# Optimization experiments

Hardware: AMD Instinct MI355X
Metric: run time of the kernel (lower is better)

## Reference

```python
import jax, jax.numpy as jnp
import numpy as np

EMBED_DIM = 1024
NUM_HEADS = 16
HEAD_DIM = EMBED_DIM // NUM_HEADS
LN_EPS = 1e-5


def setup_inputs() -> dict:
    key = jax.random.key(0)
    ks = jax.random.split(key, 10)
    B, S, D = 1, 4096, EMBED_DIM
    s = 1.0 / np.sqrt(D)
    inp = {
        'input': jax.random.normal(ks[0], (B, S, D), dtype=jnp.float32),
        'Wq': jax.random.normal(ks[1], (D, D), dtype=jnp.float32) * s,
        'bq': jnp.zeros((D,), dtype=jnp.float32),
        'Wk': jax.random.normal(ks[2], (D, D), dtype=jnp.float32) * s,
        'bk': jnp.zeros((D,), dtype=jnp.float32),
        'Wv': jax.random.normal(ks[3], (D, D), dtype=jnp.float32) * s,
        'bv': jnp.zeros((D,), dtype=jnp.float32),
        'Wo': jax.random.normal(ks[4], (D, D), dtype=jnp.float32) * s,
        'bo': jnp.zeros((D,), dtype=jnp.float32),
        'ln_gamma': jnp.ones((D,), dtype=jnp.float32),
        'ln_beta': jnp.zeros((D,), dtype=jnp.float32),
    }
    return inp


def reference(input, Wq, bq, Wk, bk, Wv, bv, Wo, bo, ln_gamma, ln_beta):
    B, S, D = input.shape
    H, Hd = NUM_HEADS, HEAD_DIM
    # projections (torch Linear: x @ W.T + b)
    q = input @ Wq.T + bq
    k = input @ Wk.T + bk
    v = input @ Wv.T + bv
    # [B, H, S, Hd]
    q = q.reshape(B, S, H, Hd).transpose(0, 2, 1, 3)
    k = k.reshape(B, S, H, Hd).transpose(0, 2, 1, 3)
    v = v.reshape(B, S, H, Hd).transpose(0, 2, 1, 3)
    scores = jnp.einsum('bhqd,bhkd->bhqk', q, k) / jnp.sqrt(jnp.float32(Hd))
    causal = jnp.tril(jnp.ones((S, S), dtype=bool))  # [S, S]
    scores = jnp.where(causal[None, None, :, :], scores, -jnp.inf)
    attn = jax.nn.softmax(scores, axis=-1)  # stable (max-subtract) internally
    out = jnp.einsum('bhqk,bhkd->bhqd', attn, v)
    out = out.transpose(0, 2, 1, 3).reshape(B, S, D)
    out = out @ Wo.T + bo
    out = out + input
    # LayerNorm
    mu = jnp.mean(out, axis=-1, keepdims=True)
    var = jnp.var(out, axis=-1, keepdims=True)
    normed = (out - mu) * jax.lax.rsqrt(var + LN_EPS)
    return normed * ln_gamma + ln_beta
```

## Files before the change

### kernel.cpp

```cpp
#include <hip/hip_runtime.h>
#include <hip/hip_bf16.h>

typedef float floatx4 __attribute__((ext_vector_type(4)));
typedef short short8 __attribute__((ext_vector_type(8)));

#define S_LEN 4096
#define D_DIM 1024
#define NHEAD 16
#define SCALE_LOG2 0.1803368801111204f

__device__ __forceinline__ void gload_lds16(const void* g, void* l) {
  __builtin_amdgcn_global_load_lds(
      (const __attribute__((address_space(1))) unsigned int*)g,
      (__attribute__((address_space(3))) unsigned int*)l, 16, 0, 0);
}

__device__ __forceinline__ unsigned short f2bf_bits(float f) {
  __hip_bfloat16 h = __float2bfloat16(f);
  return __builtin_bit_cast(unsigned short, h);
}

__global__ __launch_bounds__(256) void cvt_all(const float* __restrict__ x,
                                               const float* __restrict__ w0,
                                               const float* __restrict__ w1,
                                               const float* __restrict__ w2,
                                               const float* __restrict__ w3,
                                               unsigned short* __restrict__ xo,
                                               unsigned short* __restrict__ o0,
                                               unsigned short* __restrict__ o1,
                                               unsigned short* __restrict__ o2,
                                               unsigned short* __restrict__ o3) {
  const int bid = blockIdx.x;
  const float* in;
  unsigned short* out;
  int i;
  if (bid < 4096) {
    in = x;
    out = xo;
    i = bid * 256 + threadIdx.x;
  } else {
    const int which = (bid - 4096) >> 10;
    in = which == 0 ? w0 : which == 1 ? w1 : which == 2 ? w2 : w3;
    out = which == 0 ? o0 : which == 1 ? o1 : which == 2 ? o2 : o3;
    i = ((bid - 4096) & 1023) * 256 + threadIdx.x;
  }
  float4 v = reinterpret_cast<const float4*>(in)[i];
  ushort4 u;
  u.x = f2bf_bits(v.x);
  u.y = f2bf_bits(v.y);
  u.z = f2bf_bits(v.z);
  u.w = f2bf_bits(v.w);
  reinterpret_cast<ushort4*>(out)[i] = u;
}

__global__ __launch_bounds__(256) void gemm_qkv(const unsigned short* __restrict__ A,
                                                const unsigned short* __restrict__ WqB,
                                                const unsigned short* __restrict__ WkB,
                                                const unsigned short* __restrict__ WvB,
                                                const float* __restrict__ bq,
                                                const float* __restrict__ bk,
                                                const float* __restrict__ bv,
                                                unsigned short* __restrict__ Qo,
                                                unsigned short* __restrict__ Ko,
                                                unsigned short* __restrict__ VTo) {
  __shared__ __align__(16) unsigned short As[2][128 * 32];
  __shared__ __align__(16) unsigned short Bs[2][128 * 32];
  const int K = 1024, N = 1024, M = 4096;
  const int tid = threadIdx.x;
  const int wave = tid >> 6, lane = tid & 63;
  const int seg = blockIdx.y >> 3;
  const int m0 = blockIdx.x * 128, n0 = (blockIdx.y & 7) * 128;
  const unsigned short* B = seg == 0 ? WqB : seg == 1 ? WkB : WvB;
  const float* bias = seg == 0 ? bq : seg == 1 ? bk : bv;
  const int wr = wave >> 1, wc = wave & 1;

  floatx4 acc[4][4] = {};
  const unsigned short* Ab = A + (size_t)m0 * K;
  const unsigned short* Bb = B + (size_t)n0 * K;
  const int srow = lane >> 2, scol = (lane & 3) * 8;
  const int aRow = lane & 15, kOff = (lane >> 4) * 8;

  auto stage = [&](int buf, int k0) {
#pragma unroll
    for (int i = 0; i < 2; ++i) {
      const int c = wave * 2 + i;
      const int row = c * 16 + srow;
      gload_lds16(Ab + (size_t)row * K + k0 + scol, &As[buf][c * 512]);
      gload_lds16(Bb + (size_t)row * K + k0 + scol, &Bs[buf][c * 512]);
    }
  };

  stage(0, 0);
  int buf = 0;
  for (int k0 = 0; k0 < K; k0 += 32, buf ^= 1) {
    asm volatile("s_waitcnt vmcnt(0)" ::: "memory");
    __builtin_amdgcn_s_barrier();
    if (k0 + 32 < K) stage(buf ^ 1, k0 + 32);
    short8 af[4], bfg[4];
#pragma unroll
    for (int f = 0; f < 4; ++f) {
      af[f] =
          *reinterpret_cast<const short8*>(&As[buf][(wr * 64 + f * 16 + aRow) * 32 + kOff]);
      bfg[f] =
          *reinterpret_cast<const short8*>(&Bs[buf][(wc * 64 + f * 16 + aRow) * 32 + kOff]);
    }
#pragma unroll
    for (int fm = 0; fm < 4; ++fm)
#pragma unroll
      for (int fn = 0; fn < 4; ++fn)
        acc[fm][fn] =
            __builtin_amdgcn_mfma_f32_16x16x32_bf16(af[fm], bfg[fn], acc[fm][fn], 0, 0, 0);
  }

  const int rb = (lane >> 4) * 4, cl = lane & 15;
  const float osc = seg == 0 ? SCALE_LOG2 : 1.0f;
#pragma unroll
  for (int fm = 0; fm < 4; ++fm)
#pragma unroll
    for (int fn = 0; fn < 4; ++fn)
#pragma unroll
      for (int r = 0; r < 4; ++r) {
        const int row = m0 + wr * 64 + fm * 16 + rb + r;
        const int col = n0 + wc * 64 + fn * 16 + cl;
        const float v = (acc[fm][fn][r] + bias[col]) * osc;
        if (seg == 0)
          Qo[(size_t)row * N + col] = f2bf_bits(v);
        else if (seg == 1)
          Ko[(size_t)row * N + col] = f2bf_bits(v);
        else
          VTo[(size_t)col * M + row] = f2bf_bits(v);
      }
}

__global__ __launch_bounds__(256) void gemm_o(const unsigned short* __restrict__ A,
                                              const unsigned short* __restrict__ B,
                                              const float* __restrict__ bias,
                                              const float* __restrict__ resid,
                                              float* __restrict__ C) {
  __shared__ __align__(16) unsigned short As[2][64 * 32];
  __shared__ __align__(16) unsigned short Bs[2][128 * 32];
  const int K = 1024, N = 1024;
  const int tid = threadIdx.x;
  const int wave = tid >> 6, lane = tid & 63;
  const int m0 = blockIdx.x * 64, n0 = blockIdx.y * 128;
  const int wr = wave >> 1, wc = wave & 1;

  floatx4 acc[2][4] = {};
  const unsigned short* Ab = A + (size_t)m0 * K;
  const unsigned short* Bb = B + (size_t)n0 * K;
  const int srow = lane >> 2, scol = (lane & 3) * 8;
  const int aRow = lane & 15, kOff = (lane >> 4) * 8;

  auto stage = [&](int buf, int k0) {
#pragma unroll
    for (int i = 0; i < 3; ++i) {
      const int ci = wave * 3 + i;
      if (ci < 4) {
        const int row = ci * 16 + srow;
        gload_lds16(Ab + (size_t)row * K + k0 + scol, &As[buf][ci * 512]);
      } else {
        const int row = (ci - 4) * 16 + srow;
        gload_lds16(Bb + (size_t)row * K + k0 + scol, &Bs[buf][(ci - 4) * 512]);
      }
    }
  };

  stage(0, 0);
  int buf = 0;
  for (int k0 = 0; k0 < K; k0 += 32, buf ^= 1) {
    asm volatile("s_waitcnt vmcnt(0)" ::: "memory");
    __builtin_amdgcn_s_barrier();
    if (k0 + 32 < K) stage(buf ^ 1, k0 + 32);
    short8 af[2], bfg[4];
#pragma unroll
    for (int f = 0; f < 2; ++f)
      af[f] =
          *reinterpret_cast<const short8*>(&As[buf][(wr * 32 + f * 16 + aRow) * 32 + kOff]);
#pragma unroll
    for (int f = 0; f < 4; ++f)
      bfg[f] =
          *reinterpret_cast<const short8*>(&Bs[buf][(wc * 64 + f * 16 + aRow) * 32 + kOff]);
#pragma unroll
    for (int fm = 0; fm < 2; ++fm)
#pragma unroll
      for (int fn = 0; fn < 4; ++fn)
        acc[fm][fn] =
            __builtin_amdgcn_mfma_f32_16x16x32_bf16(af[fm], bfg[fn], acc[fm][fn], 0, 0, 0);
  }

  const int rb = (lane >> 4) * 4, cl = lane & 15;
#pragma unroll
  for (int fm = 0; fm < 2; ++fm)
#pragma unroll
    for (int fn = 0; fn < 4; ++fn)
#pragma unroll
      for (int r = 0; r < 4; ++r) {
        const int row = m0 + wr * 32 + fm * 16 + rb + r;
        const int col = n0 + wc * 64 + fn * 16 + cl;
        C[(size_t)row * N + col] =
            acc[fm][fn][r] + bias[col] + resid[(size_t)row * N + col];
      }
}

__global__ __launch_bounds__(256) void attn_fwd(const unsigned short* __restrict__ Q,
                                                const unsigned short* __restrict__ Kg,
                                                const unsigned short* __restrict__ VT,
                                                unsigned short* __restrict__ O) {
  __shared__ __align__(16) unsigned short Ks[2 * 64 * 64];
  __shared__ __align__(16) unsigned short Vs[2 * 64 * 64];
  __shared__ __align__(16) unsigned short Ps[4][16 * 64];

  const int bid = blockIdx.x;
  const int h = bid & 15;
  const int qt = 63 - (bid >> 4);
  const int q0 = qt * 64;
  const int wave = threadIdx.x >> 6, lane = threadIdx.x & 63;
  const int l15 = lane & 15, l4 = lane >> 4;
  const int q7 = l15 & 7;

  const int qrow = q0 + wave * 16 + l15;
  short8 qf[2];
#pragma unroll
  for (int ks = 0; ks < 2; ++ks)
    qf[ks] = *reinterpret_cast<const short8*>(
        &Q[(size_t)qrow * D_DIM + h * 64 + ks * 32 + l4 * 8]);

  floatx4 acco[4] = {};
  float l_run = 0.f;

  auto stageK = [&](int buf, int t) {
    const int kv0 = t * 64;
#pragma unroll
    for (int i = 0; i < 2; ++i) {
      const int seg = wave * 2 + i;
      const int c = seg * 64 + lane;
      const int r = c >> 3, jj = c & 7;
      const int sj = (jj ^ (r & 7)) * 8;
      gload_lds16(&Kg[(size_t)(kv0 + r) * D_DIM + h * 64 + sj],
                  &Ks[buf * 4096 + seg * 512]);
    }
  };
  auto stageV = [&](int buf, int t) {
    const int kv0 = t * 64;
#pragma unroll
    for (int i = 0; i < 2; ++i) {
      const int seg = wave * 2 + i;
      const int c = seg * 64 + lane;
      const int r = c >> 3, jj = c & 7;
      const int sj = (jj ^ (r & 7)) * 8;
      gload_lds16(&VT[(size_t)(h * 64 + r) * S_LEN + kv0 + sj],
                  &Vs[buf * 4096 + seg * 512]);
    }
  };

  const int ntiles = qt + 1;
  stageK(0, 0);

  for (int t = 0; t < ntiles; ++t) {
    asm volatile("s_waitcnt vmcnt(0)" ::: "memory");
    __builtin_amdgcn_s_barrier();
    if (t + 1 < ntiles) stageK((t + 1) & 1, t + 1);
    stageV(t & 1, t);

    const unsigned short* ksb = &Ks[(t & 1) * 4096];

    floatx4 accs[4] = {};
#pragma unroll
    for (int ks = 0; ks < 2; ++ks)
#pragma unroll
      for (int fn = 0; fn < 4; ++fn) {
        const int R = fn * 16 + l15;
        const int J = ks * 4 + l4;
        const short8 kf =
            *reinterpret_cast<const short8*>(&ksb[R * 64 + ((J ^ (R & 7)) * 8)]);
        accs[fn] =
            __builtin_amdgcn_mfma_f32_16x16x32_bf16(kf, qf[ks], accs[fn], 0, 0, 0);
      }

    if (t > 0) {
      const unsigned short* vsb = &Vs[((t - 1) & 1) * 4096];
#pragma unroll
      for (int kh = 0; kh < 2; ++kh) {
        const short8 pf = *reinterpret_cast<const short8*>(
            &Ps[wave][l15 * 64 + (((kh * 4 + l4) ^ q7) << 3)]);
#pragma unroll
        for (int fn = 0; fn < 4; ++fn) {
          const int R = fn * 16 + l15;
          const int J = kh * 4 + l4;
          const short8 vf =
              *reinterpret_cast<const short8*>(&vsb[R * 64 + ((J ^ (R & 7)) * 8)]);
          acco[fn] = __builtin_amdgcn_mfma_f32_16x16x32_bf16(vf, pf, acco[fn], 0, 0, 0);
        }
      }
    }

    const int kv0 = t * 64;
    float p[4][4];
    if (t == ntiles - 1) {
#pragma unroll
      for (int fn = 0; fn < 4; ++fn)
#pragma unroll
        for (int r = 0; r < 4; ++r) {
          const int ka = kv0 + fn * 16 + l4 * 4 + r;
          const float s = (ka > qrow) ? -1e30f : accs[fn][r];
          p[fn][r] = __builtin_amdgcn_exp2f(s);
        }
    } else {
#pragma unroll
      for (int fn = 0; fn < 4; ++fn)
#pragma unroll
        for (int r = 0; r < 4; ++r) p[fn][r] = __builtin_amdgcn_exp2f(accs[fn][r]);
    }
    float rs = 0.f;
#pragma unroll
    for (int fn = 0; fn < 4; ++fn)
#pragma unroll
      for (int r = 0; r < 4; ++r) rs += p[fn][r];
    l_run += rs;

#pragma unroll
    for (int fn = 0; fn < 4; ++fn) {
      const int c = 2 * fn + (l4 >> 1);
      const int off = ((c ^ q7) << 3) + ((l4 & 1) << 2);
      uint2 w;
      w.x = (unsigned)f2bf_bits(p[fn][0]) | ((unsigned)f2bf_bits(p[fn][1]) << 16);
      w.y = (unsigned)f2bf_bits(p[fn][2]) | ((unsigned)f2bf_bits(p[fn][3]) << 16);
      *reinterpret_cast<uint2*>(&Ps[wave][l15 * 64 + off]) = w;
    }
  }

  asm volatile("s_waitcnt vmcnt(0)" ::: "memory");
  __builtin_amdgcn_s_barrier();
  {
    const unsigned short* vsb = &Vs[((ntiles - 1) & 1) * 4096];
#pragma unroll
    for (int kh = 0; kh < 2; ++kh) {
      const short8 pf = *reinterpret_cast<const short8*>(
          &Ps[wave][l15 * 64 + (((kh * 4 + l4) ^ q7) << 3)]);
#pragma unroll
      for (int fn = 0; fn < 4; ++fn) {
        const int R = fn * 16 + l15;
        const int J = kh * 4 + l4;
        const short8 vf =
            *reinterpret_cast<const short8*>(&vsb[R * 64 + ((J ^ (R & 7)) * 8)]);
        acco[fn] = __builtin_amdgcn_mfma_f32_16x16x32_bf16(vf, pf, acco[fn], 0, 0, 0);
      }
    }
  }

  l_run += __shfl_xor(l_run, 16);
  l_run += __shfl_xor(l_run, 32);
  const float inv = 1.f / l_run;
#pragma unroll
  for (int fn = 0; fn < 4; ++fn)
#pragma unroll
    for (int rp = 0; rp < 2; ++rp) {
      const unsigned lo = f2bf_bits(acco[fn][2 * rp] * inv);
      const unsigned hi = f2bf_bits(acco[fn][2 * rp + 1] * inv);
      *reinterpret_cast<unsigned*>(
          &O[(size_t)qrow * D_DIM + h * 64 + fn * 16 + l4 * 4 + rp * 2]) =
          lo | (hi << 16);
    }
}

__global__ __launch_bounds__(256) void ln_kernel(const float* __restrict__ X,
                                                 const float* __restrict__ g,
                                                 const float* __restrict__ b,
                                                 float* __restrict__ Y) {
  const int row = blockIdx.x;
  const int t = threadIdx.x;
  const float4 xv = reinterpret_cast<const float4*>(X + (size_t)row * 1024)[t];
  float s = xv.x + xv.y + xv.z + xv.w;
  float s2 = xv.x * xv.x + xv.y * xv.y + xv.z * xv.z + xv.w * xv.w;
#pragma unroll
  for (int off = 1; off < 64; off <<= 1) {
    s += __shfl_xor(s, off);
    s2 += __shfl_xor(s2, off);
  }
  __shared__ float sr[4], sr2[4];
  const int wave = t >> 6, lane = t & 63;
  if (lane == 0) {
    sr[wave] = s;
    sr2[wave] = s2;
  }
  __syncthreads();
  const float S = sr[0] + sr[1] + sr[2] + sr[3];
  const float S2 = sr2[0] + sr2[1] + sr2[2] + sr2[3];
  const float mu = S * (1.f / 1024.f);
  const float var = S2 * (1.f / 1024.f) - mu * mu;
  const float rstd = rsqrtf(var + 1e-5f);
  const float4 gv = reinterpret_cast<const float4*>(g)[t];
  const float4 bv = reinterpret_cast<const float4*>(b)[t];
  float4 y;
  y.x = (xv.x - mu) * rstd * gv.x + bv.x;
  y.y = (xv.y - mu) * rstd * gv.y + bv.y;
  y.z = (xv.z - mu) * rstd * gv.z + bv.z;
  y.w = (xv.w - mu) * rstd * gv.w + bv.w;
  reinterpret_cast<float4*>(Y + (size_t)row * 1024)[t] = y;
}

extern "C" void kernel_launch(void* const* d_in, const int* in_sizes, int n_in,
                              void* d_out, int out_size, void* d_ws, size_t ws_size,
                              hipStream_t stream) {
  const float* x = (const float*)d_in[0];
  const float* Wq = (const float*)d_in[1];
  const float* bq = (const float*)d_in[2];
  const float* Wk = (const float*)d_in[3];
  const float* bk = (const float*)d_in[4];
  const float* Wv = (const float*)d_in[5];
  const float* bv = (const float*)d_in[6];
  const float* Wo = (const float*)d_in[7];
  const float* bo = (const float*)d_in[8];
  const float* gamma = (const float*)d_in[9];
  const float* beta = (const float*)d_in[10];

  char* ws = (char*)d_ws;
  const size_t MB = (size_t)1 << 20;
  unsigned short* Xb = (unsigned short*)(ws + 0);
  unsigned short* Wqb = (unsigned short*)(ws + 8 * MB);
  unsigned short* Wkb = (unsigned short*)(ws + 10 * MB);
  unsigned short* Wvb = (unsigned short*)(ws + 12 * MB);
  unsigned short* Wob = (unsigned short*)(ws + 16 * MB);
  unsigned short* Qb = (unsigned short*)(ws + 18 * MB);
  unsigned short* Kb = (unsigned short*)(ws + 26 * MB);
  unsigned short* VTb = (unsigned short*)(ws + 34 * MB);
  unsigned short* Ab = (unsigned short*)(ws + 42 * MB);
  float* proj = (float*)(ws + 0);

  cvt_all<<<8192, 256, 0, stream>>>(x, Wq, Wk, Wv, Wo, Xb, Wqb, Wkb, Wvb, Wob);

  gemm_qkv<<<dim3(32, 24), 256, 0, stream>>>(Xb, Wqb, Wkb, Wvb, bq, bk, bv, Qb, Kb,
                                             VTb);

  attn_fwd<<<dim3(1024), 256, 0, stream>>>(Qb, Kb, VTb, Ab);

  gemm_o<<<dim3(64, 8), 256, 0, stream>>>(Ab, Wob, bo, x, proj);

  ln_kernel<<<4096, 256, 0, stream>>>(proj, gamma, beta, (float*)d_out);
}
```

Baseline: 143.5 us.

## Switch attention to 32x32x16 MFMA with split-K waves and register-resident P

Rewrites the attention kernel to use 32x32x16 bf16 MFMAs. Waves are split into 2 query blocks by 2 key halves, and the probability tile stays in registers via v_permlane32_swap instead of an LDS round trip through Ps. Partial output accumulators and row sums from the two key-half waves are combined through shared memory at the end. This removes the per-tile P write/read to LDS and uses larger MFMA tiles, at the cost of an extra reduction epilogue with two block barriers.

```diff
diff --git a/kernel.cpp b/kernel.cpp
--- a/kernel.cpp
+++ b/kernel.cpp
@@ -2,7 +2,9 @@
 #include <hip/hip_bf16.h>
 
 typedef float floatx4 __attribute__((ext_vector_type(4)));
+typedef float floatx16 __attribute__((ext_vector_type(16)));
 typedef short short8 __attribute__((ext_vector_type(8)));
+typedef unsigned int uintx4 __attribute__((ext_vector_type(4)));
 
 #define S_LEN 4096
 #define D_DIM 1024
@@ -208,25 +210,27 @@
                                                 unsigned short* __restrict__ O) {
   __shared__ __align__(16) unsigned short Ks[2 * 64 * 64];
   __shared__ __align__(16) unsigned short Vs[2 * 64 * 64];
-  __shared__ __align__(16) unsigned short Ps[4][16 * 64];
+  __shared__ float Lred[64];
 
   const int bid = blockIdx.x;
   const int h = bid & 15;
   const int qt = 63 - (bid >> 4);
   const int q0 = qt * 64;
   const int wave = threadIdx.x >> 6, lane = threadIdx.x & 63;
-  const int l15 = lane & 15, l4 = lane >> 4;
-  const int q7 = l15 & 7;
-
-  const int qrow = q0 + wave * 16 + l15;
-  short8 qf[2];
-#pragma unroll
-  for (int ks = 0; ks < 2; ++ks)
-    qf[ks] = *reinterpret_cast<const short8*>(
-        &Q[(size_t)qrow * D_DIM + h * 64 + ks * 32 + l4 * 8]);
-
-  floatx4 acco[4] = {};
+  const int l31 = lane & 31, hh = lane >> 5;
+  const int kb = wave & 1, qb = wave >> 1;
+  const int sw7 = l31 & 7;
+
+  const int qrow = q0 + qb * 32 + l31;
+  short8 qf[4];
+#pragma unroll
+  for (int s = 0; s < 4; ++s)
+    qf[s] = *reinterpret_cast<const short8*>(
+        &Q[(size_t)qrow * D_DIM + h * 64 + s * 16 + hh * 8]);
+
+  floatx16 acco0 = {}, acco1 = {};
   float l_run = 0.f;
+  unsigned pfw[8];
 
   auto stageK = [&](int buf, int t) {
     const int kv0 = t * 64;
@@ -253,6 +257,35 @@
     }
   };
 
+  const int Rk = kb * 32 + l31;
+  int kaddr[4];
+#pragma unroll
+  for (int s = 0; s < 4; ++s) kaddr[s] = Rk * 64 + (((2 * s + hh) ^ sw7) * 8);
+  int vaddr0[2], vaddr1[2];
+#pragma unroll
+  for (int ks = 0; ks < 2; ++ks) {
+    vaddr0[ks] = (0 * 32 + l31) * 64 + (((4 * kb + 2 * ks + hh) ^ sw7) * 8);
+    vaddr1[ks] = (1 * 32 + l31) * 64 + (((4 * kb + 2 * ks + hh) ^ sw7) * 8);
+  }
+
+  auto do_pv = [&](const unsigned short* vsb) {
+    uintx4 u0, u1;
+    u0.x = pfw[0]; u0.y = pfw[1]; u0.z = pfw[2]; u0.w = pfw[3];
+    u1.x = pfw[4]; u1.y = pfw[5]; u1.z = pfw[6]; u1.w = pfw[7];
+    const short8 pf0 = __builtin_bit_cast(short8, u0);
+    const short8 pf1 = __builtin_bit_cast(short8, u1);
+    {
+      const short8 vf00 = *reinterpret_cast<const short8*>(&vsb[vaddr0[0]]);
+      acco0 = __builtin_amdgcn_mfma_f32_32x32x16_bf16(vf00, pf0, acco0, 0, 0, 0);
+      const short8 vf01 = *reinterpret_cast<const short8*>(&vsb[vaddr0[1]]);
+      acco0 = __builtin_amdgcn_mfma_f32_32x32x16_bf16(vf01, pf1, acco0, 0, 0, 0);
+      const short8 vf10 = *reinterpret_cast<const short8*>(&vsb[vaddr1[0]]);
+      acco1 = __builtin_amdgcn_mfma_f32_32x32x16_bf16(vf10, pf0, acco1, 0, 0, 0);
+      const short8 vf11 = *reinterpret_cast<const short8*>(&vsb[vaddr1[1]]);
+      acco1 = __builtin_amdgcn_mfma_f32_32x32x16_bf16(vf11, pf1, acco1, 0, 0, 0);
+    }
+  };
+
   const int ntiles = qt + 1;
   stageK(0, 0);
 
@@ -264,103 +297,91 @@
 
     const unsigned short* ksb = &Ks[(t & 1) * 4096];
 
-    floatx4 accs[4] = {};
-#pragma unroll
-    for (int ks = 0; ks < 2; ++ks)
-#pragma unroll
-      for (int fn = 0; fn < 4; ++fn) {
-        const int R = fn * 16 + l15;
-        const int J = ks * 4 + l4;
-        const short8 kf =
-            *reinterpret_cast<const short8*>(&ksb[R * 64 + ((J ^ (R & 7)) * 8)]);
-        accs[fn] =
-            __builtin_amdgcn_mfma_f32_16x16x32_bf16(kf, qf[ks], accs[fn], 0, 0, 0);
-      }
-
-    if (t > 0) {
-      const unsigned short* vsb = &Vs[((t - 1) & 1) * 4096];
-#pragma unroll
-      for (int kh = 0; kh < 2; ++kh) {
-        const short8 pf = *reinterpret_cast<const short8*>(
-            &Ps[wave][l15 * 64 + (((kh * 4 + l4) ^ q7) << 3)]);
-#pragma unroll
-        for (int fn = 0; fn < 4; ++fn) {
-          const int R = fn * 16 + l15;
-          const int J = kh * 4 + l4;
-          const short8 vf =
-              *reinterpret_cast<const short8*>(&vsb[R * 64 + ((J ^ (R & 7)) * 8)]);
-          acco[fn] = __builtin_amdgcn_mfma_f32_16x16x32_bf16(vf, pf, acco[fn], 0, 0, 0);
-        }
-      }
-    }
+    floatx16 accs = {};
+#pragma unroll
+    for (int s = 0; s < 4; ++s) {
+      const short8 kf = *reinterpret_cast<const short8*>(&ksb[kaddr[s]]);
+      accs = __builtin_amdgcn_mfma_f32_32x32x16_bf16(kf, qf[s], accs, 0, 0, 0);
+    }
+
+    if (t > 0) do_pv(&Vs[((t - 1) & 1) * 4096]);
 
     const int kv0 = t * 64;
-    float p[4][4];
+    float p[16];
     if (t == ntiles - 1) {
 #pragma unroll
-      for (int fn = 0; fn < 4; ++fn)
-#pragma unroll
-        for (int r = 0; r < 4; ++r) {
-          const int ka = kv0 + fn * 16 + l4 * 4 + r;
-          const float s = (ka > qrow) ? -1e30f : accs[fn][r];
-          p[fn][r] = __builtin_amdgcn_exp2f(s);
-        }
+      for (int reg = 0; reg < 16; ++reg) {
+        const int ka = kv0 + kb * 32 + (reg & 3) + 8 * (reg >> 2) + 4 * hh;
+        const float s = (ka > qrow) ? -1e30f : accs[reg];
+        p[reg] = __builtin_amdgcn_exp2f(s);
+      }
     } else {
 #pragma unroll
-      for (int fn = 0; fn < 4; ++fn)
-#pragma unroll
-        for (int r = 0; r < 4; ++r) p[fn][r] = __builtin_amdgcn_exp2f(accs[fn][r]);
+      for (int reg = 0; reg < 16; ++reg) p[reg] = __builtin_amdgcn_exp2f(accs[reg]);
     }
     float rs = 0.f;
 #pragma unroll
-    for (int fn = 0; fn < 4; ++fn)
-#pragma unroll
-      for (int r = 0; r < 4; ++r) rs += p[fn][r];
+    for (int reg = 0; reg < 16; ++reg) rs += p[reg];
     l_run += rs;
 
-#pragma unroll
-    for (int fn = 0; fn < 4; ++fn) {
-      const int c = 2 * fn + (l4 >> 1);
-      const int off = ((c ^ q7) << 3) + ((l4 & 1) << 2);
-      uint2 w;
-      w.x = (unsigned)f2bf_bits(p[fn][0]) | ((unsigned)f2bf_bits(p[fn][1]) << 16);
-      w.y = (unsigned)f2bf_bits(p[fn][2]) | ((unsigned)f2bf_bits(p[fn][3]) << 16);
-      *reinterpret_cast<uint2*>(&Ps[wave][l15 * 64 + off]) = w;
+    {
+      unsigned w0 = (unsigned)f2bf_bits(p[0]) | ((unsigned)f2bf_bits(p[1]) << 16);
+      unsigned w1 = (unsigned)f2bf_bits(p[2]) | ((unsigned)f2bf_bits(p[3]) << 16);
+      unsigned w2 = (unsigned)f2bf_bits(p[4]) | ((unsigned)f2bf_bits(p[5]) << 16);
+      unsigned w3 = (unsigned)f2bf_bits(p[6]) | ((unsigned)f2bf_bits(p[7]) << 16);
+      unsigned w4 = (unsigned)f2bf_bits(p[8]) | ((unsigned)f2bf_bits(p[9]) << 16);
+      unsigned w5 = (unsigned)f2bf_bits(p[10]) | ((unsigned)f2bf_bits(p[11]) << 16);
+      unsigned w6 = (unsigned)f2bf_bits(p[12]) | ((unsigned)f2bf_bits(p[13]) << 16);
+      unsigned w7 = (unsigned)f2bf_bits(p[14]) | ((unsigned)f2bf_bits(p[15]) << 16);
+      asm volatile("v_permlane32_swap_b32 %0, %1" : "+v"(w0), "+v"(w2));
+      asm volatile("v_permlane32_swap_b32 %0, %1" : "+v"(w1), "+v"(w3));
+      asm volatile("v_permlane32_swap_b32 %0, %1" : "+v"(w4), "+v"(w6));
+      asm volatile("v_permlane32_swap_b32 %0, %1" : "+v"(w5), "+v"(w7));
+      pfw[0] = w0; pfw[1] = w1; pfw[2] = w2; pfw[3] = w3;
+      pfw[4] = w4; pfw[5] = w5; pfw[6] = w6; pfw[7] = w7;
     }
   }
 
   asm volatile("s_waitcnt vmcnt(0)" ::: "memory");
   __builtin_amdgcn_s_barrier();
-  {
-    const unsigned short* vsb = &Vs[((ntiles - 1) & 1) * 4096];
-#pragma unroll
-    for (int kh = 0; kh < 2; ++kh) {
-      const short8 pf = *reinterpret_cast<const short8*>(
-          &Ps[wave][l15 * 64 + (((kh * 4 + l4) ^ q7) << 3)]);
-#pragma unroll
-      for (int fn = 0; fn < 4; ++fn) {
-        const int R = fn * 16 + l15;
-        const int J = kh * 4 + l4;
-        const short8 vf =
-            *reinterpret_cast<const short8*>(&vsb[R * 64 + ((J ^ (R & 7)) * 8)]);
-        acco[fn] = __builtin_amdgcn_mfma_f32_16x16x32_bf16(vf, pf, acco[fn], 0, 0, 0);
-      }
-    }
-  }
-
-  l_run += __shfl_xor(l_run, 16);
+  do_pv(&Vs[((ntiles - 1) & 1) * 4096]);
+
   l_run += __shfl_xor(l_run, 32);
-  const float inv = 1.f / l_run;
-#pragma unroll
-  for (int fn = 0; fn < 4; ++fn)
-#pragma unroll
-    for (int rp = 0; rp < 2; ++rp) {
-      const unsigned lo = f2bf_bits(acco[fn][2 * rp] * inv);
-      const unsigned hi = f2bf_bits(acco[fn][2 * rp + 1] * inv);
-      *reinterpret_cast<unsigned*>(
-          &O[(size_t)qrow * D_DIM + h * 64 + fn * 16 + l4 * 4 + rp * 2]) =
-          lo | (hi << 16);
-    }
+
+  __syncthreads();
+  float* scr = reinterpret_cast<float*>(Ks);
+  if (kb == 1) {
+#pragma unroll
+    for (int reg = 0; reg < 16; ++reg) {
+      const int row = (reg & 3) + 8 * (reg >> 2) + 4 * hh;
+      scr[(qb * 2 + 0) * 1024 + row * 32 + l31] = acco0[reg];
+      scr[(qb * 2 + 1) * 1024 + row * 32 + l31] = acco1[reg];
+    }
+    if (lane < 32) Lred[qb * 32 + l31] = l_run;
+  }
+  __syncthreads();
+  if (kb == 0) {
+    const float inv = 1.f / (l_run + Lred[qb * 32 + l31]);
+#pragma unroll
+    for (int reg8 = 0; reg8 < 8; ++reg8) {
+      const int ra = 2 * reg8, rb2 = 2 * reg8 + 1;
+      const int rowa = (ra & 3) + 8 * (ra >> 2) + 4 * hh;
+      {
+        const float va = (acco0[ra] + scr[(qb * 2 + 0) * 1024 + rowa * 32 + l31]) * inv;
+        const float vb =
+            (acco0[rb2] + scr[(qb * 2 + 0) * 1024 + (rowa + 1) * 32 + l31]) * inv;
+        const unsigned pk = (unsigned)f2bf_bits(va) | ((unsigned)f2bf_bits(vb) << 16);
+        *reinterpret_cast<unsigned*>(&O[(size_t)qrow * D_DIM + h * 64 + 0 + rowa]) = pk;
+      }
+      {
+        const float va = (acco1[ra] + scr[(qb * 2 + 1) * 1024 + rowa * 32 + l31]) * inv;
+        const float vb =
+            (acco1[rb2] + scr[(qb * 2 + 1) * 1024 + (rowa + 1) * 32 + l31]) * inv;
+        const unsigned pk = (unsigned)f2bf_bits(va) | ((unsigned)f2bf_bits(vb) << 16);
+        *reinterpret_cast<unsigned*>(&O[(size_t)qrow * D_DIM + h * 64 + 32 + rowa]) = pk;
+      }
+    }
+  }
 }
 
 __global__ __launch_bounds__(256) void ln_kernel(const float* __restrict__ X,
```

New measurement: 151.5 us. 1.06x slower.
